# Kernel optimization log

Measured on AMD Instinct MI355X. Metric: run time of the kernel, lower is better.

Reference implementation:

```python
import jax, jax.numpy as jnp
import numpy as np

SQRT3 = 3.0 ** 0.5
MAX_RADIUS = 5.0
NUM_BASIS = 10
NUM_NEIGHBORS = 15.0
# e3nn soft_one_hot_linspace 'smooth_finite' prefactor: 1.14136 * e^2
SMOOTH_C = 1.14136 * float(np.exp(2.0))


def _sus(x):
    # smooth compactly-supported bump helper: exp(-1/x) for x>0 else 0
    return jnp.where(x > 0.0, jnp.exp(-1.0 / jnp.where(x > 0.0, x, 1.0)), 0.0)


def _soft_one_hot(x):
    # e3nn soft_one_hot_linspace(start=0, end=5, number=10, basis='smooth_finite', cutoff=True)
    values = jnp.linspace(0.0, MAX_RADIUS, NUM_BASIS + 2)[1:-1]  # interior knots
    step = MAX_RADIUS / (NUM_BASIS + 1)
    diff = (x[:, None] - values) / step  # [E, 10]
    return SMOOTH_C * _sus(diff + 1.0) * _sus(1.0 - diff)


def _sh_l1(v, normalize):
    # spherical harmonics up to lmax=1, 'component' normalization.
    # e3nn l=1 component ordering is (y, z, x), each scaled by sqrt(3).
    if normalize:
        v = v / (jnp.linalg.norm(v, axis=-1, keepdims=True) + 1e-9)
    x, y, z = v[..., 0], v[..., 1], v[..., 2]
    return jnp.stack([jnp.ones_like(x), SQRT3 * y, SQRT3 * z, SQRT3 * x], axis=-1)


def setup_inputs() -> dict:
    key = jax.random.key(0)
    ks = jax.random.split(key, 12)
    N, E, G, Fin, D, L, A, H = 100000, 800000, 64, 16, 32, 3, 4, 64
    pos = jax.random.normal(ks[0], (N, 3), jnp.float32) * 1.5
    x = jax.random.normal(ks[1], (N, Fin), jnp.float32)
    orientation = jax.random.uniform(ks[2], (G, 2), jnp.float32)
    edge_src = jax.random.randint(ks[3], (E,), 0, N)
    edge_dst = jax.random.randint(ks[4], (E,), 0, N)
    batch = jnp.sort(jax.random.randint(ks[5], (N,), 0, G))
    W_embed = jax.random.normal(ks[6], (Fin, D), jnp.float32)
    W_tp = jax.random.normal(ks[7], (L, D, A, D), jnp.float32)
    W_fc1 = jax.random.normal(ks[8], (L, NUM_BASIS, H), jnp.float32)
    W_fc2 = jax.random.normal(ks[9], (L, H, 1), jnp.float32)
    W_dec = jax.random.normal(ks[10], (D, A), jnp.float32)
    return {"pos": pos, "x": x, "orientation": orientation, "W_embed": W_embed,
            "W_tp": W_tp, "W_fc1": W_fc1, "W_fc2": W_fc2, "W_dec": W_dec,
            "edge_src": edge_src, "edge_dst": edge_dst, "batch": batch}


def reference(pos, x, orientation, W_embed, W_tp, W_fc1, W_fc2, W_dec,
              edge_src, edge_dst, batch):
    N = x.shape[0]
    G = orientation.shape[0]
    D = W_embed.shape[1]
    A = W_tp.shape[2]
    H = W_fc1.shape[2]

    edge_vec = pos[edge_src] - pos[edge_dst]            # [E, 3]
    edge_len = jnp.linalg.norm(edge_vec, axis=-1)       # [E]
    edge_attr = _sh_l1(edge_vec, True)                  # [E, 4]
    edge_len_emb = _soft_one_hot(edge_len) * (NUM_BASIS ** 0.5)  # [E, 10]

    h = x @ W_embed  # embedding o3.Linear -> [N, D]
    tp_norm = 1.0 / float(np.sqrt(D * A))
    fc1_norm = 1.0 / float(np.sqrt(NUM_BASIS))
    fc2_norm = 1.0 / float(np.sqrt(H))
    agg_norm = 1.0 / float(np.sqrt(NUM_NEIGHBORS))

    for l in range(W_tp.shape[0]):  # fixed small layer count
        h_src = h[edge_src]  # gather [E, D]
        # fully-connected tensor product (bilinear): contract node features with
        # weights first to keep the big intermediate at [E, A, D]
        t = jnp.einsum('ei,iak->eak', h_src, W_tp[l])
        ang = jnp.einsum('eak,ea->ek', t, edge_attr) * tp_norm  # [E, D]
        hid = jax.nn.silu(edge_len_emb @ W_fc1[l] * fc1_norm)   # [E, 64]
        rad = hid @ W_fc2[l] * fc2_norm                          # [E, 1]
        msg = ang * rad                                          # [E, D]
        agg = jax.ops.segment_sum(msg, edge_dst, num_segments=N)
        h = h + agg * agg_norm  # residual

    # graph mean pooling
    gsum = jax.ops.segment_sum(h, batch, num_segments=G)
    cnt = jax.ops.segment_sum(jnp.ones((N,), jnp.float32), batch, num_segments=G)
    graph = gsum / jnp.maximum(cnt, 1.0)[:, None]  # [G, D]

    sh_coeffs = graph @ W_dec  # decoder o3.Linear -> [G, 4]
    theta, phi = orientation[..., 0], orientation[..., 1]
    q = jnp.stack([jnp.sin(theta) * jnp.cos(phi),
                   jnp.sin(theta) * jnp.sin(phi),
                   jnp.cos(theta)], axis=-1)  # unit vectors [G, 3]
    sh_q = _sh_l1(q, False)
    return (sh_coeffs * sh_q).sum(axis=-1)  # [G]
```

## Files before the change

kernel.cpp:

```cpp
#include <hip/hip_runtime.h>


constexpr int Dk  = 32;
constexpr int Hk  = 64;
constexpr int NBk = 10;
constexpr int Lk  = 3;
constexpr int FinK = 16;
constexpr int TAB = 8192;
constexpr int SCB = 256;

__device__ __forceinline__ float sus(float x) {
    return x > 0.f ? __expf(-1.f / x) : 0.f;
}

__device__ __forceinline__ unsigned pack_bf16_rne(float a, float b) {
    unsigned ua = __float_as_uint(a), ub = __float_as_uint(b);
    ua += 0x7FFFu + ((ua >> 16) & 1u);
    ub += 0x7FFFu + ((ub >> 16) & 1u);
    return (ua >> 16) | (ub & 0xFFFF0000u);
}

__global__ __launch_bounds__(256) void radial_tab_k(
    const float* __restrict__ Wfc1, const float* __restrict__ Wfc2,
    float* __restrict__ rtab)
{
    int l = blockIdx.y;
    __shared__ float sW1[NBk * Hk];
    __shared__ float sW2[Hk];
    for (int j = threadIdx.x; j < NBk * Hk; j += blockDim.x) sW1[j] = Wfc1[l * NBk * Hk + j];
    for (int j = threadIdx.x; j < Hk; j += blockDim.x) sW2[j] = Wfc2[l * Hk + j];
    __syncthreads();

    int i = blockIdx.x * blockDim.x + threadIdx.x;
    if (i > TAB) return;
    float len = 5.f * (float)i / (float)TAB;
    const float C_EMB = (float)(1.14136 * 7.3890560989306495);
    float t = len * 2.2f;
    float emb[NBk];
#pragma unroll
    for (int j = 0; j < NBk; j++) {
        float d1 = t - (float)j;
        float d2 = (float)(j + 2) - t;
        emb[j] = C_EMB * sus(d1) * sus(d2);
    }
    const float C_OUT = (float)(0.125 * 0.08838834764831845 * 0.2581988897471611);
    float r = 0.f;
    for (int j = 0; j < Hk; j++) {
        float a = 0.f;
#pragma unroll
        for (int b = 0; b < NBk; b++) a += emb[b] * sW1[b * Hk + j];
        float sg = 1.f / (1.f + __expf(-a));
        r += a * sg * sW2[j];
    }
    rtab[l * (TAB + 1) + i] = r * C_OUT;
}

__global__ __launch_bounds__(256) void hist_k(
    const int* __restrict__ edst, int* __restrict__ deg, int E)
{
    int e = blockIdx.x * blockDim.x + threadIdx.x;
    if (e < E) atomicAdd(&deg[edst[e]], 1);
}

__global__ __launch_bounds__(SCB) void scan1_k(
    const int* __restrict__ deg, int* __restrict__ incl,
    int* __restrict__ bsum, int N)
{
    __shared__ int s[SCB];
    int g = blockIdx.x * SCB + threadIdx.x;
    s[threadIdx.x] = (g < N) ? deg[g] : 0;
    __syncthreads();
    for (int off = 1; off < SCB; off <<= 1) {
        int t = (threadIdx.x >= off) ? s[threadIdx.x - off] : 0;
        __syncthreads();
        s[threadIdx.x] += t;
        __syncthreads();
    }
    if (g < N) incl[g] = s[threadIdx.x];
    if (threadIdx.x == SCB - 1) bsum[blockIdx.x] = s[threadIdx.x];
}

__global__ __launch_bounds__(512) void scan2_k(int* __restrict__ bsum, int nb)
{
    __shared__ int s[512];
    s[threadIdx.x] = (threadIdx.x < nb) ? bsum[threadIdx.x] : 0;
    __syncthreads();
    for (int off = 1; off < 512; off <<= 1) {
        int t = (threadIdx.x >= off) ? s[threadIdx.x - off] : 0;
        __syncthreads();
        s[threadIdx.x] += t;
        __syncthreads();
    }
    if (threadIdx.x < nb) bsum[threadIdx.x] = s[threadIdx.x];
}

__global__ __launch_bounds__(SCB) void scan3_k(
    const int* __restrict__ deg, const int* __restrict__ incl,
    const int* __restrict__ bsum, int* __restrict__ row_ptr,
    int* __restrict__ cur, int N, int E)
{
    int g = blockIdx.x * SCB + threadIdx.x;
    if (g < N) {
        int off = (blockIdx.x > 0) ? bsum[blockIdx.x - 1] : 0;
        int excl = incl[g] - deg[g] + off;
        row_ptr[g] = excl;
        cur[g] = excl;
    }
    if (g == 0) row_ptr[N] = E;
}

__global__ __launch_bounds__(256) void edge_pre(
    const float* __restrict__ pos, const int* __restrict__ esrc,
    const int* __restrict__ edst, const float* __restrict__ rtab,
    int* __restrict__ cur, int* __restrict__ esrc2,
    float4* __restrict__ attr2, float* __restrict__ cfac2, int E)
{
    int e = blockIdx.x * blockDim.x + threadIdx.x;
    if (e >= E) return;
    int s = esrc[e], d = edst[e];
    float vx = pos[3 * s + 0] - pos[3 * d + 0];
    float vy = pos[3 * s + 1] - pos[3 * d + 1];
    float vz = pos[3 * s + 2] - pos[3 * d + 2];
    float len = sqrtf(vx * vx + vy * vy + vz * vz);
    float inv = 1.f / (len + 1e-9f);
    const float S3 = 1.7320508075688772f;

    float xx = fminf(len * ((float)TAB / 5.f), (float)TAB);
    int i = min((int)xx, TAB - 1);
    float f = xx - (float)i;

    int p = atomicAdd(&cur[d], 1);
    esrc2[p] = s;
    attr2[p] = make_float4(1.f, S3 * vy * inv, S3 * vz * inv, S3 * vx * inv);
#pragma unroll
    for (int l = 0; l < Lk; l++) {
        float a = rtab[l * (TAB + 1) + i];
        float b = rtab[l * (TAB + 1) + i + 1];
        cfac2[(size_t)l * E + p] = a + (b - a) * f;
    }
}

__global__ __launch_bounds__(256) void embed_k(
    const float* __restrict__ x, const float* __restrict__ We,
    float* __restrict__ h, int N)
{
    __shared__ float sW[FinK * Dk];
    for (int i = threadIdx.x; i < FinK * Dk; i += blockDim.x) sW[i] = We[i];
    __syncthreads();
    int tid = blockIdx.x * blockDim.x + threadIdx.x;
    int n = tid >> 5, k = tid & 31;
    if (n >= N) return;
    float acc = 0.f;
#pragma unroll
    for (int i = 0; i < FinK; i++) acc += x[n * FinK + i] * sW[i * Dk + k];
    h[n * Dk + k] = acc;
}

__global__ __launch_bounds__(256) void tp_gemm(
    const float* __restrict__ h, const float* __restrict__ Wl,
    unsigned* __restrict__ HpU, int N)
{
    int tid = blockIdx.x * blockDim.x + threadIdx.x;
    int n = tid >> 5, k = tid & 31;
    if (n >= N) return;
    float hv = h[(size_t)n * Dk + k];
    float a0 = 0.f, a1 = 0.f, a2 = 0.f, a3 = 0.f;
#pragma unroll
    for (int i = 0; i < Dk; i++) {
        float hb = __shfl(hv, i, 32);
        a0 += hb * Wl[i * 128 + 0 * 32 + k];
        a1 += hb * Wl[i * 128 + 1 * 32 + k];
        a2 += hb * Wl[i * 128 + 2 * 32 + k];
        a3 += hb * Wl[i * 128 + 3 * 32 + k];
    }
    unsigned* o = HpU + (size_t)n * 64;
    o[k]      = pack_bf16_rne(a0, a1);
    o[32 + k] = pack_bf16_rne(a2, a3);
}

__global__ __launch_bounds__(256) void agg_k(
    const unsigned* __restrict__ HpU, const float4* __restrict__ attr2,
    const float* __restrict__ cl, const int* __restrict__ esrc2,
    const int* __restrict__ row_ptr, float* __restrict__ h, int N)
{
    int tid = blockIdx.x * blockDim.x + threadIdx.x;
    int n = tid >> 5, k = tid & 31;
    if (n >= N) return;
    int r0 = row_ptr[n], r1 = row_ptr[n + 1];
    float acc = 0.f;
    for (int i = r0; i < r1; ++i) {
        int s = esrc2[i];
        float4 a = attr2[i];
        float c = cl[i];
        const unsigned* hp = HpU + (size_t)s * 64;
        unsigned u01 = hp[k], u23 = hp[32 + k];
        float h0 = __uint_as_float(u01 << 16);
        float h1 = __uint_as_float(u01 & 0xFFFF0000u);
        float h2 = __uint_as_float(u23 << 16);
        float h3 = __uint_as_float(u23 & 0xFFFF0000u);
        acc += c * (a.x * h0 + a.y * h1 + a.z * h2 + a.w * h3);
    }
    h[(size_t)n * Dk + k] += acc;
}

constexpr int POOL_NPB = 512;
__global__ __launch_bounds__(256) void pool_k(
    const float* __restrict__ h, const int* __restrict__ batch,
    float* __restrict__ gsum, float* __restrict__ cnt, int N)
{
    int k = threadIdx.x & 31;
    int row = threadIdx.x >> 5;
    int start = blockIdx.x * POOL_NPB;
    int end = min(start + POOL_NPB, N);
    int curg = -1;
    float acc = 0.f, cacc = 0.f;
    for (int n = start + row; n < end; n += 8) {
        int g = batch[n];
        float v = h[(size_t)n * Dk + k];
        if (g != curg) {
            if (curg >= 0) {
                unsafeAtomicAdd(&gsum[curg * Dk + k], acc);
                if (k == 0) unsafeAtomicAdd(&cnt[curg], cacc);
            }
            curg = g; acc = 0.f; cacc = 0.f;
        }
        acc += v; cacc += 1.f;
    }
    if (curg >= 0) {
        unsafeAtomicAdd(&gsum[curg * Dk + k], acc);
        if (k == 0) unsafeAtomicAdd(&cnt[curg], cacc);
    }
}

__global__ __launch_bounds__(64) void final_k(
    const float* __restrict__ gsum, const float* __restrict__ cnt,
    const float* __restrict__ Wdec, const float* __restrict__ orient,
    float* __restrict__ out, int G)
{
    int g = blockIdx.x * blockDim.x + threadIdx.x;
    if (g >= G) return;
    float ic = 1.f / fmaxf(cnt[g], 1.f);
    float c0 = 0.f, c1 = 0.f, c2 = 0.f, c3 = 0.f;
#pragma unroll
    for (int i = 0; i < Dk; i++) {
        float gv = gsum[g * Dk + i] * ic;
        c0 += gv * Wdec[i * 4 + 0];
        c1 += gv * Wdec[i * 4 + 1];
        c2 += gv * Wdec[i * 4 + 2];
        c3 += gv * Wdec[i * 4 + 3];
    }
    float th = orient[g * 2 + 0], ph = orient[g * 2 + 1];
    float st = sinf(th), ct = cosf(th), sp = sinf(ph), cp = cosf(ph);
    float qx = st * cp, qy = st * sp, qz = ct;
    const float S3 = 1.7320508075688772f;
    out[g] = c0 + c1 * S3 * qy + c2 * S3 * qz + c3 * S3 * qx;
}

extern "C" void kernel_launch(void* const* d_in, const int* in_sizes, int n_in,
                              void* d_out, int out_size, void* d_ws, size_t ws_size,
                              hipStream_t stream) {
    const float* pos     = (const float*)d_in[0];
    const float* x       = (const float*)d_in[1];
    const float* orient  = (const float*)d_in[2];
    const float* W_embed = (const float*)d_in[3];
    const float* W_tp    = (const float*)d_in[4];
    const float* W_fc1   = (const float*)d_in[5];
    const float* W_fc2   = (const float*)d_in[6];
    const float* W_dec   = (const float*)d_in[7];
    const int*   esrc    = (const int*)d_in[8];
    const int*   edst    = (const int*)d_in[9];
    const int*   batch   = (const int*)d_in[10];

    const int N = in_sizes[0] / 3;
    const int E = in_sizes[8];
    const int G = in_sizes[2] / 2;
    const int NB = (N + SCB - 1) / SCB;

    float*    ws     = (float*)d_ws;
    float4*   attr2  = (float4*)ws;
    float*    cfac2  = ws + (size_t)4 * E;
    float*    h      = cfac2 + (size_t)3 * E;
    unsigned* HpU    = (unsigned*)(h + (size_t)Dk * N);
    float*    gsum   = (float*)(HpU + (size_t)64 * N);
    float*    cnt    = gsum + (size_t)Dk * G;
    float*    rtab   = cnt + G;
    int*      esrc2  = (int*)(rtab + 3 * (TAB + 1));
    int*      deg    = esrc2 + E;
    int*      incl   = deg + N;
    int*      row_ptr= incl + N;
    int*      cur    = row_ptr + (N + 1);
    int*      bsum   = cur + N;

    hipMemsetAsync(deg, 0, (size_t)N * sizeof(int), stream);
    hipMemsetAsync(gsum, 0, (size_t)(Dk * G + G) * sizeof(float), stream);

    {
        dim3 grid((TAB + 1 + 255) / 256, Lk);
        radial_tab_k<<<grid, 256, 0, stream>>>(W_fc1, W_fc2, rtab);
    }
    hist_k<<<(E + 255) / 256, 256, 0, stream>>>(edst, deg, E);
    scan1_k<<<NB, SCB, 0, stream>>>(deg, incl, bsum, N);
    scan2_k<<<1, 512, 0, stream>>>(bsum, NB);
    scan3_k<<<NB, SCB, 0, stream>>>(deg, incl, bsum, row_ptr, cur, N, E);

    edge_pre<<<(E + 255) / 256, 256, 0, stream>>>(
        pos, esrc, edst, rtab, cur, esrc2, attr2, cfac2, E);
    embed_k<<<(N * 32 + 255) / 256, 256, 0, stream>>>(x, W_embed, h, N);

    for (int l = 0; l < Lk; l++) {
        tp_gemm<<<(N * 32 + 255) / 256, 256, 0, stream>>>(
            h, W_tp + (size_t)l * 128 * 32 / 32 * 32, HpU, N);
        agg_k<<<(N * 32 + 255) / 256, 256, 0, stream>>>(
            HpU, attr2, cfac2 + (size_t)l * E, esrc2, row_ptr, h, N);
    }

    pool_k<<<(N + POOL_NPB - 1) / POOL_NPB, 256, 0, stream>>>(h, batch, gsum, cnt, N);
    final_k<<<(G + 63) / 64, 64, 0, stream>>>(gsum, cnt, W_dec, orient, (float*)d_out, G);
}
```

Measured before the change: 571.8 us.

## Split edge preprocessing into placement and coalesced fill, use SoA edge attributes

Edge preprocessing is split into two kernels. One uses atomics to build a permutation, and the other fills CSR-ordered arrays sequentially by position, so the writes coalesce. The edge attributes move from a float4 array to three separate float arrays, and the constant 1 component is dropped. The packed bf16 node projections are interleaved so that agg_k reads one uint2 per lane instead of two scattered uint loads. This adds an extra kernel launch, a permutation array, and gathers of esrc, edst and pos through the permutation.

New measurement: 587.7 us. +2.8%, slower.

```diff
diff --git a/kernel.cpp b/kernel.cpp
--- a/kernel.cpp
+++ b/kernel.cpp
@@ -109,14 +109,27 @@
     if (g == 0) row_ptr[N] = E;
 }
 
-__global__ __launch_bounds__(256) void edge_pre(
-    const float* __restrict__ pos, const int* __restrict__ esrc,
-    const int* __restrict__ edst, const float* __restrict__ rtab,
-    int* __restrict__ cur, int* __restrict__ esrc2,
-    float4* __restrict__ attr2, float* __restrict__ cfac2, int E)
+__global__ __launch_bounds__(256) void place_k(
+    const int* __restrict__ edst, int* __restrict__ cur,
+    int* __restrict__ perm, int E)
 {
     int e = blockIdx.x * blockDim.x + threadIdx.x;
     if (e >= E) return;
+    int p = atomicAdd(&cur[edst[e]], 1);
+    perm[p] = e;
+}
+
+__global__ __launch_bounds__(256) void fill_k(
+    const int* __restrict__ perm, const int* __restrict__ esrc,
+    const int* __restrict__ edst, const float* __restrict__ pos,
+    const float* __restrict__ rtab,
+    int* __restrict__ esrc2, float* __restrict__ aY,
+    float* __restrict__ aZ, float* __restrict__ aX,
+    float* __restrict__ cfac2, int E)
+{
+    int p = blockIdx.x * blockDim.x + threadIdx.x;
+    if (p >= E) return;
+    int e = perm[p];
     int s = esrc[e], d = edst[e];
     float vx = pos[3 * s + 0] - pos[3 * d + 0];
     float vy = pos[3 * s + 1] - pos[3 * d + 1];
@@ -129,9 +142,10 @@
     int i = min((int)xx, TAB - 1);
     float f = xx - (float)i;
 
-    int p = atomicAdd(&cur[d], 1);
     esrc2[p] = s;
-    attr2[p] = make_float4(1.f, S3 * vy * inv, S3 * vz * inv, S3 * vx * inv);
+    aY[p] = S3 * vy * inv;
+    aZ[p] = S3 * vz * inv;
+    aX[p] = S3 * vx * inv;
 #pragma unroll
     for (int l = 0; l < Lk; l++) {
         float a = rtab[l * (TAB + 1) + i];
@@ -174,12 +188,13 @@
         a3 += hb * Wl[i * 128 + 3 * 32 + k];
     }
     unsigned* o = HpU + (size_t)n * 64;
-    o[k]      = pack_bf16_rne(a0, a1);
-    o[32 + k] = pack_bf16_rne(a2, a3);
+    o[2 * k]     = pack_bf16_rne(a0, a1);
+    o[2 * k + 1] = pack_bf16_rne(a2, a3);
 }
 
 __global__ __launch_bounds__(256) void agg_k(
-    const unsigned* __restrict__ HpU, const float4* __restrict__ attr2,
+    const unsigned* __restrict__ HpU, const float* __restrict__ aY,
+    const float* __restrict__ aZ, const float* __restrict__ aX,
     const float* __restrict__ cl, const int* __restrict__ esrc2,
     const int* __restrict__ row_ptr, float* __restrict__ h, int N)
 {
@@ -190,15 +205,14 @@
     float acc = 0.f;
     for (int i = r0; i < r1; ++i) {
         int s = esrc2[i];
-        float4 a = attr2[i];
+        float ay = aY[i], az = aZ[i], ax = aX[i];
         float c = cl[i];
-        const unsigned* hp = HpU + (size_t)s * 64;
-        unsigned u01 = hp[k], u23 = hp[32 + k];
-        float h0 = __uint_as_float(u01 << 16);
-        float h1 = __uint_as_float(u01 & 0xFFFF0000u);
-        float h2 = __uint_as_float(u23 << 16);
-        float h3 = __uint_as_float(u23 & 0xFFFF0000u);
-        acc += c * (a.x * h0 + a.y * h1 + a.z * h2 + a.w * h3);
+        uint2 u = ((const uint2*)(HpU + (size_t)s * 64))[k];
+        float h0 = __uint_as_float(u.x << 16);
+        float h1 = __uint_as_float(u.x & 0xFFFF0000u);
+        float h2 = __uint_as_float(u.y << 16);
+        float h3 = __uint_as_float(u.y & 0xFFFF0000u);
+        acc += c * (h0 + ay * h1 + az * h2 + ax * h3);
     }
     h[(size_t)n * Dk + k] += acc;
 }
@@ -277,15 +291,18 @@
     const int NB = (N + SCB - 1) / SCB;
 
     float*    ws     = (float*)d_ws;
-    float4*   attr2  = (float4*)ws;
-    float*    cfac2  = ws + (size_t)4 * E;
-    float*    h      = cfac2 + (size_t)3 * E;
+    float*    cfac2  = ws;
+    float*    aY     = cfac2 + (size_t)3 * E;
+    float*    aZ     = aY + E;
+    float*    aX     = aZ + E;
+    float*    h      = aX + E;
     unsigned* HpU    = (unsigned*)(h + (size_t)Dk * N);
     float*    gsum   = (float*)(HpU + (size_t)64 * N);
     float*    cnt    = gsum + (size_t)Dk * G;
     float*    rtab   = cnt + G;
     int*      esrc2  = (int*)(rtab + 3 * (TAB + 1));
-    int*      deg    = esrc2 + E;
+    int*      perm   = esrc2 + E;
+    int*      deg    = perm + E;
     int*      incl   = deg + N;
     int*      row_ptr= incl + N;
     int*      cur    = row_ptr + (N + 1);
@@ -303,15 +320,16 @@
     scan2_k<<<1, 512, 0, stream>>>(bsum, NB);
     scan3_k<<<NB, SCB, 0, stream>>>(deg, incl, bsum, row_ptr, cur, N, E);
 
-    edge_pre<<<(E + 255) / 256, 256, 0, stream>>>(
-        pos, esrc, edst, rtab, cur, esrc2, attr2, cfac2, E);
+    place_k<<<(E + 255) / 256, 256, 0, stream>>>(edst, cur, perm, E);
+    fill_k<<<(E + 255) / 256, 256, 0, stream>>>(
+        perm, esrc, edst, pos, rtab, esrc2, aY, aZ, aX, cfac2, E);
     embed_k<<<(N * 32 + 255) / 256, 256, 0, stream>>>(x, W_embed, h, N);
 
     for (int l = 0; l < Lk; l++) {
         tp_gemm<<<(N * 32 + 255) / 256, 256, 0, stream>>>(
-            h, W_tp + (size_t)l * 128 * 32 / 32 * 32, HpU, N);
+            h, W_tp + (size_t)l * Dk * 4 * Dk, HpU, N);
         agg_k<<<(N * 32 + 255) / 256, 256, 0, stream>>>(
-            HpU, attr2, cfac2 + (size_t)l * E, esrc2, row_ptr, h, N);
+            HpU, aY, aZ, aX, cfac2 + (size_t)l * E, esrc2, row_ptr, h, N);
     }
 
     pool_k<<<(N + POOL_NPB - 1) / POOL_NPB, 256, 0, stream>>>(h, batch, gsum, cnt, N);
```
